# Optimization experiments

Measured on AMD Instinct MI355X. Metric: run time of the kernel, lower is better.

## Reference

```python
import jax, jax.numpy as jnp
import numpy as np
from jax import lax

BN_EPS = 1e-5


def _conv_block(x, w, b):
    # conv k=3 pad=1 (NCHW), relu, maxpool 2x2 stride 2 (floor)
    y = lax.conv_general_dilated(x, w, (1, 1), [(1, 1), (1, 1)],
                                 dimension_numbers=('NCHW', 'OIHW', 'NCHW'))
    y = jax.nn.relu(y + b[None, :, None, None])
    y = lax.reduce_window(y, -jnp.inf, lax.max, (1, 1, 2, 2), (1, 1, 2, 2), 'VALID')
    return y


def _batchnorm_train(x, g, b):
    # BatchNorm2d in train mode: biased batch stats over (N,H,W)
    m = jnp.mean(x, axis=(0, 2, 3), keepdims=True)
    v = jnp.mean(jnp.square(x - m), axis=(0, 2, 3), keepdims=True)
    return g[None, :, None, None] * (x - m) * lax.rsqrt(v + BN_EPS) + b[None, :, None, None]


def setup_inputs() -> dict:
    key = jax.random.key(0)
    ks = jax.random.split(key, 16)
    B = 4096
    s = lambda k, shape, fan: jax.random.normal(k, shape, jnp.float32) * (1.0 / np.sqrt(fan))
    return {
        'x':   jax.random.normal(ks[0], (B, 1, 28, 28), jnp.float32),
        'cw1': s(ks[1], (32, 1, 3, 3), 9),    'cb1': jnp.zeros((32,), jnp.float32),
        'cw2': s(ks[2], (32, 32, 3, 3), 288), 'cb2': jnp.zeros((32,), jnp.float32),
        'cw3': s(ks[3], (32, 32, 3, 3), 288), 'cb3': jnp.zeros((32,), jnp.float32),
        'bn_g': jnp.ones((32,), jnp.float32), 'bn_b': jnp.zeros((32,), jnp.float32),
        'pw1': s(ks[4], (288, 128), 288), 'pb1': jnp.zeros((128,), jnp.float32),
        'pw2': s(ks[5], (128, 128), 128), 'pb2': jnp.zeros((128,), jnp.float32),
        'pw3': s(ks[6], (128, 3), 128),   'pb3': jnp.zeros((3,), jnp.float32),
        'ew1': s(ks[7], (3, 288, 128), 288), 'eb1': jnp.zeros((3, 128), jnp.float32),
        'ew2': s(ks[8], (3, 128, 128), 128), 'eb2': jnp.zeros((3, 128), jnp.float32),
        'ew3': s(ks[9], (3, 128, 10), 128),  'eb3': jnp.zeros((3, 10), jnp.float32),
    }


def _select_linear(h, oh, ew, eb):
    # per-example expert Linear: compute all 3 tiny experts, pick via one-hot
    y = jnp.einsum('bi,eio->beo', h, ew) + eb[None]  # [B,3,out]
    return jnp.einsum('beo,be->bo', y, oh)


def reference(x, cw1, cb1, cw2, cb2, cw3, cb3, bn_g, bn_b,
              pw1, pb1, pw2, pb2, pw3, pb3,
              ew1, eb1, ew2, eb2, ew3, eb3):
    # conv stack
    y = _conv_block(x, cw1, cb1)
    y = _conv_block(y, cw2, cb2)
    y = _conv_block(y, cw3, cb3)
    y = _batchnorm_train(y, bn_g, bn_b)
    y = y.reshape(y.shape[0], -1)  # [B, 288]

    # ActorCritic approx policy MLP (288 -> 128 -> 128 -> 3), greedy action
    h = jax.nn.relu(y @ pw1 + pb1)
    h = jax.nn.relu(h @ pw2 + pb2)
    logits = h @ pw3 + pb3
    actions = jnp.argmax(logits, axis=-1)          # [B] int, routing decision
    oh = jax.nn.one_hot(actions, 3, dtype=y.dtype)  # [B,3]

    # three SelectionLayers, same per-example routing decision
    y = _select_linear(y, oh, ew1, eb1)
    y = _select_linear(y, oh, ew2, eb2)
    y = _select_linear(y, oh, ew3, eb3)  # [B,10]
    return y, actions
```

## Files before the change

### kernel.cpp

```cpp
#include <hip/hip_runtime.h>

__global__ __launch_bounds__(256) void repack_kernel(
    const float* __restrict__ cw2, const float* __restrict__ cw3,
    float* __restrict__ packed2, float* __restrict__ packed3)
{
    int t = blockIdx.x * 256 + threadIdx.x;
    if (t < 9216) {
        int oc = t & 31, r = t >> 5;
        packed2[t] = cw2[oc * 288 + r];
    } else {
        int t2 = t - 9216;
        int oc = t2 & 31, r = t2 >> 5;
        packed3[t2] = cw3[oc * 288 + r];
    }
}

__global__ __launch_bounds__(256)
void fused_conv_kernel(
    const float* __restrict__ x,
    const float* __restrict__ cw1, const float* __restrict__ cb1,
    const float* __restrict__ packed2, const float* __restrict__ cb2,
    const float* __restrict__ packed3, const float* __restrict__ cb3,
    float* __restrict__ out3)
{
    const int img = blockIdx.x;
    const int tid = threadIdx.x;

    __shared__ float A[2304];
    __shared__ float B[10368];
    __shared__ float b2s[32], b3s[32];

    float* xs1 = A;
    float* w1s = A + 900;
    float* b1s = A + 1188;
    float* wck = A;
    float* xs2 = B;
    float* sc  = B;
    float* xs3 = B + 6384;

    for (int i = tid; i < 900;   i += 256) xs1[i] = 0.f;
    for (int i = tid; i < 10368; i += 256) B[i] = 0.f;
    __syncthreads();

    for (int i = tid; i < 784; i += 256) {
        int yy = i / 28, xx = i % 28;
        xs1[(yy + 1) * 30 + xx + 1] = x[img * 784 + i];
    }
    for (int i = tid; i < 288; i += 256) {
        int oc = i & 31, tap = i >> 5;
        w1s[i] = cw1[oc * 9 + tap];
    }
    if (tid < 32) { b1s[tid] = cb1[tid]; b2s[tid] = cb2[tid]; b3s[tid] = cb3[tid]; }
    __syncthreads();

    {
        const int c1 = tid & 31;
        float w1r[9];
        #pragma unroll
        for (int t = 0; t < 9; t++) w1r[t] = w1s[t * 32 + c1];
        const float bias1 = b1s[c1];
        for (int o = tid; o < 32 * 196; o += 256) {
            int p = o >> 5;
            int py = p / 14, px = p % 14;
            int base = (2 * py) * 30 + 2 * px;
            float P[16];
            #pragma unroll
            for (int r = 0; r < 4; r++) {
                float2 u0 = *(const float2*)&xs1[base + r * 30];
                float2 u1 = *(const float2*)&xs1[base + r * 30 + 2];
                P[r * 4 + 0] = u0.x; P[r * 4 + 1] = u0.y;
                P[r * 4 + 2] = u1.x; P[r * 4 + 3] = u1.y;
            }
            float a00 = 0.f, a01 = 0.f, a10 = 0.f, a11 = 0.f;
            #pragma unroll
            for (int ky = 0; ky < 3; ky++)
                #pragma unroll
                for (int kx = 0; kx < 3; kx++) {
                    float w = w1r[ky * 3 + kx];
                    a00 = fmaf(P[ky * 4 + kx],           w, a00);
                    a01 = fmaf(P[ky * 4 + kx + 1],       w, a01);
                    a10 = fmaf(P[(ky + 1) * 4 + kx],     w, a10);
                    a11 = fmaf(P[(ky + 1) * 4 + kx + 1], w, a11);
                }
            float v = fmaxf(fmaxf(fmaxf(a00, a01), fmaxf(a10, a11)) + bias1, 0.f);
            xs2[c1 * 324 + (py + 1) * 20 + (px + 1)] = v;
        }
    }

    const int g  = tid >> 7;
    const int u  = tid & 127;
    const int cb = u & 7, R = u >> 3;
    const int oc0 = cb * 4;
    const bool act2 = (u < 112);

    float acc[4][14];
    #pragma unroll
    for (int a = 0; a < 4; a++)
        #pragma unroll
        for (int c = 0; c < 14; c++) acc[a][c] = 0.f;

    float pf[9];
    #pragma unroll
    for (int k = 0; k < 9; k++) pf[k] = packed2[tid + k * 256];

    for (int ch = 0; ch < 4; ch++) {
        __syncthreads();
        #pragma unroll
        for (int k = 0; k < 9; k++) wck[tid + k * 256] = pf[k];
        if (ch < 3) {
            #pragma unroll
            for (int k = 0; k < 9; k++) pf[k] = packed2[(ch + 1) * 2304 + tid + k * 256];
        }
        __syncthreads();
        if (act2) {
            #pragma unroll 2
            for (int d = 0; d < 4; d++) {
                const int ld = g * 4 + d;
                const int ic = ch * 8 + ld;
                const float* wd = &wck[ld * 288 + oc0];
                const int pb = ic * 324;
                #pragma unroll
                for (int ky = 0; ky < 3; ky++) {
                    const int rb = pb + (R + ky) * 20;
                    float row[16];
                    #pragma unroll
                    for (int q = 0; q < 4; q++) {
                        const float4 t = *(const float4*)&xs2[rb + q * 4];
                        row[q * 4 + 0] = t.x; row[q * 4 + 1] = t.y;
                        row[q * 4 + 2] = t.z; row[q * 4 + 3] = t.w;
                    }
                    const float4 wa = *(const float4*)&wd[(ky * 3 + 0) * 32];
                    const float4 wb = *(const float4*)&wd[(ky * 3 + 1) * 32];
                    const float4 wc = *(const float4*)&wd[(ky * 3 + 2) * 32];
                    #pragma unroll
                    for (int c = 0; c < 14; c++) {
                        acc[0][c] = fmaf(row[c],     wa.x, acc[0][c]);
                        acc[1][c] = fmaf(row[c],     wa.y, acc[1][c]);
                        acc[2][c] = fmaf(row[c],     wa.z, acc[2][c]);
                        acc[3][c] = fmaf(row[c],     wa.w, acc[3][c]);
                        acc[0][c] = fmaf(row[c + 1], wb.x, acc[0][c]);
                        acc[1][c] = fmaf(row[c + 1], wb.y, acc[1][c]);
                        acc[2][c] = fmaf(row[c + 1], wb.z, acc[2][c]);
                        acc[3][c] = fmaf(row[c + 1], wb.w, acc[3][c]);
                        acc[0][c] = fmaf(row[c + 2], wc.x, acc[0][c]);
                        acc[1][c] = fmaf(row[c + 2], wc.y, acc[1][c]);
                        acc[2][c] = fmaf(row[c + 2], wc.z, acc[2][c]);
                        acc[3][c] = fmaf(row[c + 2], wc.w, acc[3][c]);
                    }
                }
            }
        }
    }

    __syncthreads();
    if (g == 1 && act2) {
        #pragma unroll
        for (int a = 0; a < 4; a++)
            #pragma unroll
            for (int c = 0; c < 14; c++) sc[u * 57 + a * 14 + c] = acc[a][c];
    }
    __syncthreads();
    if (g == 0 && act2) {
        #pragma unroll
        for (int a = 0; a < 4; a++)
            #pragma unroll
            for (int c = 0; c < 14; c++) acc[a][c] += sc[u * 57 + a * 14 + c];
    }
    __syncthreads();

    for (int i = tid; i < 2880; i += 256) xs3[i] = 0.f;
    float hm[4][7];
    if (g == 0 && act2) {
        #pragma unroll
        for (int a = 0; a < 4; a++)
            #pragma unroll
            for (int c = 0; c < 7; c++)
                hm[a][c] = fmaxf(acc[a][2 * c], acc[a][2 * c + 1]);
        if (R & 1) {
            #pragma unroll
            for (int a = 0; a < 4; a++)
                #pragma unroll
                for (int c = 0; c < 7; c++) sc[u * 29 + a * 7 + c] = hm[a][c];
        }
    }
    __syncthreads();
    if (g == 0 && act2 && !(R & 1)) {
        const int py = R >> 1;
        #pragma unroll
        for (int a = 0; a < 4; a++)
            #pragma unroll
            for (int c = 0; c < 7; c++) {
                float v = fmaxf(hm[a][c], sc[(u + 8) * 29 + a * 7 + c]);
                v = fmaxf(v + b2s[oc0 + a], 0.f);
                xs3[(oc0 + a) * 90 + (py + 1) * 10 + (c + 1)] = v;
            }
    }

    const int u3 = tid & 127;
    const bool act3 = (u3 < 72);
    const int cq3 = u3 & 7, pos = u3 >> 3;
    const int oc30 = cq3 * 4;
    const int py3 = pos / 3, px3 = pos % 3;
    const int base3 = (2 * py3) * 10 + 2 * px3;

    float a3[4][4];
    #pragma unroll
    for (int a = 0; a < 4; a++)
        #pragma unroll
        for (int q = 0; q < 4; q++) a3[a][q] = 0.f;

    float pg[9];
    #pragma unroll
    for (int k = 0; k < 9; k++) pg[k] = packed3[tid + k * 256];

    for (int ch = 0; ch < 4; ch++) {
        __syncthreads();
        #pragma unroll
        for (int k = 0; k < 9; k++) wck[tid + k * 256] = pg[k];
        if (ch < 3) {
            #pragma unroll
            for (int k = 0; k < 9; k++) pg[k] = packed3[(ch + 1) * 2304 + tid + k * 256];
        }
        __syncthreads();
        if (act3) {
            #pragma unroll 2
            for (int d = 0; d < 4; d++) {
                const int ld = g * 4 + d;
                const int ic = ch * 8 + ld;
                const float* xp = &xs3[ic * 90 + base3];
                float P[16];
                #pragma unroll
                for (int r = 0; r < 4; r++) {
                    float2 u0 = *(const float2*)&xp[r * 10];
                    float2 u1 = *(const float2*)&xp[r * 10 + 2];
                    P[r * 4 + 0] = u0.x; P[r * 4 + 1] = u0.y;
                    P[r * 4 + 2] = u1.x; P[r * 4 + 3] = u1.y;
                }
                const float* wd = &wck[ld * 288 + oc30];
                #pragma unroll
                for (int tap = 0; tap < 9; tap++) {
                    const int ky = tap / 3, kx = tap % 3;
                    const float4 wv = *(const float4*)&wd[tap * 32];
                    const float x00 = P[ky * 4 + kx];
                    const float x01 = P[ky * 4 + kx + 1];
                    const float x10 = P[(ky + 1) * 4 + kx];
                    const float x11 = P[(ky + 1) * 4 + kx + 1];
                    a3[0][0] = fmaf(x00, wv.x, a3[0][0]); a3[0][1] = fmaf(x01, wv.x, a3[0][1]);
                    a3[0][2] = fmaf(x10, wv.x, a3[0][2]); a3[0][3] = fmaf(x11, wv.x, a3[0][3]);
                    a3[1][0] = fmaf(x00, wv.y, a3[1][0]); a3[1][1] = fmaf(x01, wv.y, a3[1][1]);
                    a3[1][2] = fmaf(x10, wv.y, a3[1][2]); a3[1][3] = fmaf(x11, wv.y, a3[1][3]);
                    a3[2][0] = fmaf(x00, wv.z, a3[2][0]); a3[2][1] = fmaf(x01, wv.z, a3[2][1]);
                    a3[2][2] = fmaf(x10, wv.z, a3[2][2]); a3[2][3] = fmaf(x11, wv.z, a3[2][3]);
                    a3[3][0] = fmaf(x00, wv.w, a3[3][0]); a3[3][1] = fmaf(x01, wv.w, a3[3][1]);
                    a3[3][2] = fmaf(x10, wv.w, a3[3][2]); a3[3][3] = fmaf(x11, wv.w, a3[3][3]);
                }
            }
        }
    }

    __syncthreads();
    if (g == 1 && act3) {
        #pragma unroll
        for (int a = 0; a < 4; a++)
            #pragma unroll
            for (int q = 0; q < 4; q++) sc[u3 * 17 + a * 4 + q] = a3[a][q];
    }
    __syncthreads();
    if (g == 0 && act3) {
        #pragma unroll
        for (int a = 0; a < 4; a++)
            #pragma unroll
            for (int q = 0; q < 4; q++) a3[a][q] += sc[u3 * 17 + a * 4 + q];
        float4 res;
        float* r = (float*)&res;
        #pragma unroll
        for (int a = 0; a < 4; a++) {
            float v = fmaxf(fmaxf(a3[a][0], a3[a][1]), fmaxf(a3[a][2], a3[a][3]));
            r[a] = fmaxf(v + b3s[oc30 + a], 0.f);
        }
        *(float4*)&out3[img * 288 + pos * 32 + oc30] = res;
    }
}

__global__ __launch_bounds__(256) void bn_part_kernel(
    const float* __restrict__ out3, float* __restrict__ pS, float* __restrict__ pSS)
{
    const int blk = blockIdx.x;
    const int c = threadIdx.x & 31, ml = threadIdx.x >> 5;
    float s = 0.f, ss = 0.f;
    const int base = blk * 576 + ml;
    for (int k = 0; k < 72; k++) {
        float v = out3[(base + k * 8) * 32 + c];
        s += v; ss = fmaf(v, v, ss);
    }
    __shared__ float rs[256], rss[256];
    rs[threadIdx.x] = s; rss[threadIdx.x] = ss;
    __syncthreads();
    if (threadIdx.x < 32) {
        float S = 0.f, SS = 0.f;
        #pragma unroll
        for (int m = 0; m < 8; m++) { S += rs[threadIdx.x + 32 * m]; SS += rss[threadIdx.x + 32 * m]; }
        pS[blk * 32 + threadIdx.x] = S;
        pSS[blk * 32 + threadIdx.x] = SS;
    }
}

__global__ __launch_bounds__(64) void bn_final_kernel(
    const float* __restrict__ pS, const float* __restrict__ pSS,
    const float* __restrict__ bng, const float* __restrict__ bnb,
    float* __restrict__ stats)
{
    int c = threadIdx.x;
    if (c < 32) {
        float S = 0.f, SS = 0.f;
        for (int b = 0; b < 64; b++) { S += pS[b * 32 + c]; SS += pSS[b * 32 + c]; }
        const float inv_n = 1.f / (4096.f * 9.f);
        float mean = S * inv_n;
        float var = SS * inv_n - mean * mean;
        float a = bng[c] * rsqrtf(var + 1e-5f);
        stats[c] = a;
        stats[32 + c] = bnb[c] - a * mean;
    }
}

__global__ __launch_bounds__(256) void mlp_select_kernel(
    const float* __restrict__ out3, const float* __restrict__ stats,
    const float* __restrict__ pw1, const float* __restrict__ pb1,
    const float* __restrict__ pw2, const float* __restrict__ pb2,
    const float* __restrict__ pw3, const float* __restrict__ pb3,
    const float* __restrict__ ew1, const float* __restrict__ eb1,
    const float* __restrict__ ew2, const float* __restrict__ eb2,
    const float* __restrict__ ew3, const float* __restrict__ eb3,
    float* __restrict__ out)
{
    const int tid = threadIdx.x;
    const int img0 = blockIdx.x * 8;

    __shared__ float ysT[288 * 14];
    __shared__ float hAT[128 * 14];
    __shared__ float hBT[128 * 14];
    __shared__ float lg[24];
    __shared__ int   acts[8];
    __shared__ float sa[32], sb[32];

    if (tid < 32) { sa[tid] = stats[tid]; sb[tid] = stats[32 + tid]; }
    __syncthreads();

    for (int it = 0; it < 3; it++) {
        int i4 = it * 256 + tid;
        if (i4 < 576) {
            int e = i4 / 72, jq = i4 - e * 72;
            float4 v = *(const float4*)&out3[(img0 + e) * 288 + jq * 4];
            int j = jq * 4;
            ysT[(j + 0) * 14 + e] = fmaf(sa[(j + 0) & 31], v.x, sb[(j + 0) & 31]);
            ysT[(j + 1) * 14 + e] = fmaf(sa[(j + 1) & 31], v.y, sb[(j + 1) & 31]);
            ysT[(j + 2) * 14 + e] = fmaf(sa[(j + 2) & 31], v.z, sb[(j + 2) & 31]);
            ysT[(j + 3) * 14 + e] = fmaf(sa[(j + 3) & 31], v.w, sb[(j + 3) & 31]);
        }
    }
    __syncthreads();

    const int n2 = tid & 63, eT = tid >> 6, e0 = eT * 2;
    float acc[2][2];

    #pragma unroll
    for (int e = 0; e < 2; e++) { acc[e][0] = pb1[n2 * 2]; acc[e][1] = pb1[n2 * 2 + 1]; }
    for (int k = 0; k < 288; k++) {
        int i = (k & 31) * 9 + (k >> 5);
        float2 w = *(const float2*)&pw1[i * 128 + n2 * 2];
        float2 yv = *(const float2*)&ysT[k * 14 + e0];
        acc[0][0] = fmaf(yv.x, w.x, acc[0][0]); acc[0][1] = fmaf(yv.x, w.y, acc[0][1]);
        acc[1][0] = fmaf(yv.y, w.x, acc[1][0]); acc[1][1] = fmaf(yv.y, w.y, acc[1][1]);
    }
    #pragma unroll
    for (int e = 0; e < 2; e++)
        #pragma unroll
        for (int d = 0; d < 2; d++)
            hAT[(n2 * 2 + d) * 14 + e0 + e] = fmaxf(acc[e][d], 0.f);
    __syncthreads();

    #pragma unroll
    for (int e = 0; e < 2; e++) { acc[e][0] = pb2[n2 * 2]; acc[e][1] = pb2[n2 * 2 + 1]; }
    for (int k = 0; k < 128; k++) {
        float2 w = *(const float2*)&pw2[k * 128 + n2 * 2];
        float2 hv = *(const float2*)&hAT[k * 14 + e0];
        acc[0][0] = fmaf(hv.x, w.x, acc[0][0]); acc[0][1] = fmaf(hv.x, w.y, acc[0][1]);
        acc[1][0] = fmaf(hv.y, w.x, acc[1][0]); acc[1][1] = fmaf(hv.y, w.y, acc[1][1]);
    }
    #pragma unroll
    for (int e = 0; e < 2; e++)
        #pragma unroll
        for (int d = 0; d < 2; d++)
            hBT[(n2 * 2 + d) * 14 + e0 + e] = fmaxf(acc[e][d], 0.f);
    __syncthreads();

    if (tid < 24) {
        int e = tid / 3, o = tid - e * 3;
        float s = pb3[o];
        for (int k = 0; k < 128; k++) s = fmaf(hBT[k * 14 + e], pw3[k * 3 + o], s);
        lg[e * 3 + o] = s;
    }
    __syncthreads();
    if (tid < 8) {
        float l0 = lg[tid * 3], l1 = lg[tid * 3 + 1], l2 = lg[tid * 3 + 2];
        int a = 0; float best = l0;
        if (l1 > best) { best = l1; a = 1; }
        if (l2 > best) { best = l2; a = 2; }
        acts[tid] = a;
        out[4096 * 10 + img0 + tid] = (float)a;
    }
    __syncthreads();

    const int a0 = acts[e0], a1 = acts[e0 + 1];

    {
        const float* wb0 = ew1 + a0 * 36864;
        const float* wb1 = ew1 + a1 * 36864;
        #pragma unroll
        for (int e = 0; e < 2; e++) { acc[e][0] = 0.f; acc[e][1] = 0.f; }
        for (int k = 0; k < 288; k++) {
            int i = (k & 31) * 9 + (k >> 5);
            float2 wA = *(const float2*)&wb0[i * 128 + n2 * 2];
            float2 wB = *(const float2*)&wb1[i * 128 + n2 * 2];
            float2 yv = *(const float2*)&ysT[k * 14 + e0];
            acc[0][0] = fmaf(yv.x, wA.x, acc[0][0]); acc[0][1] = fmaf(yv.x, wA.y, acc[0][1]);
            acc[1][0] = fmaf(yv.y, wB.x, acc[1][0]); acc[1][1] = fmaf(yv.y, wB.y, acc[1][1]);
        }
        hAT[(n2 * 2 + 0) * 14 + e0 + 0] = acc[0][0] + eb1[a0 * 128 + n2 * 2 + 0];
        hAT[(n2 * 2 + 1) * 14 + e0 + 0] = acc[0][1] + eb1[a0 * 128 + n2 * 2 + 1];
        hAT[(n2 * 2 + 0) * 14 + e0 + 1] = acc[1][0] + eb1[a1 * 128 + n2 * 2 + 0];
        hAT[(n2 * 2 + 1) * 14 + e0 + 1] = acc[1][1] + eb1[a1 * 128 + n2 * 2 + 1];
    }
    __syncthreads();

    {
        const float* wb0 = ew2 + a0 * 16384;
        const float* wb1 = ew2 + a1 * 16384;
        #pragma unroll
        for (int e = 0; e < 2; e++) { acc[e][0] = 0.f; acc[e][1] = 0.f; }
        for (int k = 0; k < 128; k++) {
            float2 wA = *(const float2*)&wb0[k * 128 + n2 * 2];
            float2 wB = *(const float2*)&wb1[k * 128 + n2 * 2];
            float2 hv = *(const float2*)&hAT[k * 14 + e0];
            acc[0][0] = fmaf(hv.x, wA.x, acc[0][0]); acc[0][1] = fmaf(hv.x, wA.y, acc[0][1]);
            acc[1][0] = fmaf(hv.y, wB.x, acc[1][0]); acc[1][1] = fmaf(hv.y, wB.y, acc[1][1]);
        }
        hBT[(n2 * 2 + 0) * 14 + e0 + 0] = acc[0][0] + eb2[a0 * 128 + n2 * 2 + 0];
        hBT[(n2 * 2 + 1) * 14 + e0 + 0] = acc[0][1] + eb2[a0 * 128 + n2 * 2 + 1];
        hBT[(n2 * 2 + 0) * 14 + e0 + 1] = acc[1][0] + eb2[a1 * 128 + n2 * 2 + 0];
        hBT[(n2 * 2 + 1) * 14 + e0 + 1] = acc[1][1] + eb2[a1 * 128 + n2 * 2 + 1];
    }
    __syncthreads();

    if (tid < 80) {
        int e = tid / 10, o = tid - e * 10;
        int a = acts[e];
        float s = eb3[a * 10 + o];
        const float* w3 = &ew3[a * 1280];
        for (int k = 0; k < 128; k++) s = fmaf(hBT[k * 14 + e], w3[k * 10 + o], s);
        out[(img0 + e) * 10 + o] = s;
    }
}

extern "C" void kernel_launch(void* const* d_in, const int* in_sizes, int n_in,
                              void* d_out, int out_size, void* d_ws, size_t ws_size,
                              hipStream_t stream)
{
    const float* x   = (const float*)d_in[0];
    const float* cw1 = (const float*)d_in[1];
    const float* cb1 = (const float*)d_in[2];
    const float* cw2 = (const float*)d_in[3];
    const float* cb2 = (const float*)d_in[4];
    const float* cw3 = (const float*)d_in[5];
    const float* cb3 = (const float*)d_in[6];
    const float* bng = (const float*)d_in[7];
    const float* bnb = (const float*)d_in[8];
    const float* pw1 = (const float*)d_in[9];
    const float* pb1 = (const float*)d_in[10];
    const float* pw2 = (const float*)d_in[11];
    const float* pb2 = (const float*)d_in[12];
    const float* pw3 = (const float*)d_in[13];
    const float* pb3 = (const float*)d_in[14];
    const float* ew1 = (const float*)d_in[15];
    const float* eb1 = (const float*)d_in[16];
    const float* ew2 = (const float*)d_in[17];
    const float* eb2 = (const float*)d_in[18];
    const float* ew3 = (const float*)d_in[19];
    const float* eb3 = (const float*)d_in[20];

    float* out     = (float*)d_out;
    float* out3    = (float*)d_ws;
    float* pS      = out3 + 4096 * 288;
    float* pSS     = pS + 2048;
    float* stats   = pSS + 2048;
    float* packed2 = stats + 64;
    float* packed3 = packed2 + 9216;

    repack_kernel<<<72, 256, 0, stream>>>(cw2, cw3, packed2, packed3);
    fused_conv_kernel<<<4096, 256, 0, stream>>>(x, cw1, cb1, packed2, cb2, packed3, cb3, out3);
    bn_part_kernel<<<64, 256, 0, stream>>>(out3, pS, pSS);
    bn_final_kernel<<<1, 64, 0, stream>>>(pS, pSS, bng, bnb, stats);
    mlp_select_kernel<<<512, 256, 0, stream>>>(out3, stats,
                                               pw1, pb1, pw2, pb2, pw3, pb3,
                                               ew1, eb1, ew2, eb2, ew3, eb3, out);
}
```

Measured before the change: 492.5 us.

## Shrink conv2 LDS footprint with swizzled 16-wide rows and smaller weight chunks

Cuts the padded conv2 input plane from a 20-float to a 16-float row stride and XOR-style rotates the float4 column groups per row to avoid LDS bank conflicts. Weight staging for conv2 now uses 8 chunks of 4 input channels instead of 4 chunks of 8, and conv3 weights and the pooling scratch are relocated into the freed B region. The goal is lower shared memory per block so more blocks can be resident per CU, and fewer bank conflicts. In exchange it adds twice as many barrier rounds in conv2, plus index arithmetic and buffer aliasing that have to stay correct.

```diff
diff --git a/kernel.cpp b/kernel.cpp
--- a/kernel.cpp
+++ b/kernel.cpp
@@ -26,20 +26,22 @@
     const int img = blockIdx.x;
     const int tid = threadIdx.x;
 
-    __shared__ float A[2304];
-    __shared__ float B[10368];
+    __shared__ float A[1220];
+    __shared__ float B[8320];
     __shared__ float b2s[32], b3s[32];
 
-    float* xs1 = A;
-    float* w1s = A + 900;
-    float* b1s = A + 1188;
-    float* wck = A;
-    float* xs2 = B;
-    float* sc  = B;
-    float* xs3 = B + 6384;
-
-    for (int i = tid; i < 900;   i += 256) xs1[i] = 0.f;
-    for (int i = tid; i < 10368; i += 256) B[i] = 0.f;
+    float* xs1  = A;
+    float* w1s  = A + 900;
+    float* b1s  = A + 1188;
+    float* wck2 = A;
+    float* xs2  = B;
+    float* sc   = B;
+    float* xs3  = B + 1280;
+    float* wck3 = B + 4160;
+    float* sc2  = B + 5073;
+
+    for (int i = tid; i < 900;  i += 256) xs1[i] = 0.f;
+    for (int i = tid; i < 8320; i += 256) B[i] = 0.f;
     __syncthreads();
 
     for (int i = tid; i < 784; i += 256) {
@@ -83,7 +85,8 @@
                     a11 = fmaf(P[(ky + 1) * 4 + kx + 1], w, a11);
                 }
             float v = fmaxf(fmaxf(fmaxf(a00, a01), fmaxf(a10, a11)) + bias1, 0.f);
-            xs2[c1 * 324 + (py + 1) * 20 + (px + 1)] = v;
+            int r = py + 1, col = px + 1;
+            xs2[c1 * 260 + r * 16 + ((((col >> 2) + r) & 3) << 2) + (col & 3)] = v;
         }
     }
 
@@ -99,33 +102,43 @@
         #pragma unroll
         for (int c = 0; c < 14; c++) acc[a][c] = 0.f;
 
-    float pf[9];
-    #pragma unroll
-    for (int k = 0; k < 9; k++) pf[k] = packed2[tid + k * 256];
-
-    for (int ch = 0; ch < 4; ch++) {
+    float pf[5];
+    #pragma unroll
+    for (int k = 0; k < 5; k++) {
+        int idx = tid + k * 256;
+        pf[k] = (idx < 1152) ? packed2[idx] : 0.f;
+    }
+
+    for (int ch = 0; ch < 8; ch++) {
         __syncthreads();
         #pragma unroll
-        for (int k = 0; k < 9; k++) wck[tid + k * 256] = pf[k];
-        if (ch < 3) {
-            #pragma unroll
-            for (int k = 0; k < 9; k++) pf[k] = packed2[(ch + 1) * 2304 + tid + k * 256];
+        for (int k = 0; k < 5; k++) {
+            int idx = tid + k * 256;
+            if (idx < 1152) wck2[idx] = pf[k];
+        }
+        if (ch < 7) {
+            #pragma unroll
+            for (int k = 0; k < 5; k++) {
+                int idx = tid + k * 256;
+                pf[k] = (idx < 1152) ? packed2[(ch + 1) * 1152 + idx] : 0.f;
+            }
         }
         __syncthreads();
         if (act2) {
-            #pragma unroll 2
-            for (int d = 0; d < 4; d++) {
-                const int ld = g * 4 + d;
-                const int ic = ch * 8 + ld;
-                const float* wd = &wck[ld * 288 + oc0];
-                const int pb = ic * 324;
+            #pragma unroll
+            for (int d = 0; d < 2; d++) {
+                const int ld = g * 2 + d;
+                const int ic = ch * 4 + ld;
+                const float* wd = &wck2[ld * 288 + oc0];
+                const int pb = ic * 260;
                 #pragma unroll
                 for (int ky = 0; ky < 3; ky++) {
-                    const int rb = pb + (R + ky) * 20;
+                    const int rp = R + ky;
+                    const int rb = pb + rp * 16;
                     float row[16];
                     #pragma unroll
                     for (int q = 0; q < 4; q++) {
-                        const float4 t = *(const float4*)&xs2[rb + q * 4];
+                        const float4 t = *(const float4*)&xs2[rb + (((q + rp) & 3) << 2)];
                         row[q * 4 + 0] = t.x; row[q * 4 + 1] = t.y;
                         row[q * 4 + 2] = t.z; row[q * 4 + 3] = t.w;
                     }
@@ -180,7 +193,7 @@
             #pragma unroll
             for (int a = 0; a < 4; a++)
                 #pragma unroll
-                for (int c = 0; c < 7; c++) sc[u * 29 + a * 7 + c] = hm[a][c];
+                for (int c = 0; c < 7; c++) sc2[u * 29 + a * 7 + c] = hm[a][c];
         }
     }
     __syncthreads();
@@ -190,7 +203,7 @@
         for (int a = 0; a < 4; a++)
             #pragma unroll
             for (int c = 0; c < 7; c++) {
-                float v = fmaxf(hm[a][c], sc[(u + 8) * 29 + a * 7 + c]);
+                float v = fmaxf(hm[a][c], sc2[(u + 8) * 29 + a * 7 + c]);
                 v = fmaxf(v + b2s[oc0 + a], 0.f);
                 xs3[(oc0 + a) * 90 + (py + 1) * 10 + (c + 1)] = v;
             }
@@ -216,7 +229,7 @@
     for (int ch = 0; ch < 4; ch++) {
         __syncthreads();
         #pragma unroll
-        for (int k = 0; k < 9; k++) wck[tid + k * 256] = pg[k];
+        for (int k = 0; k < 9; k++) wck3[tid + k * 256] = pg[k];
         if (ch < 3) {
             #pragma unroll
             for (int k = 0; k < 9; k++) pg[k] = packed3[(ch + 1) * 2304 + tid + k * 256];
@@ -236,7 +249,7 @@
                     P[r * 4 + 0] = u0.x; P[r * 4 + 1] = u0.y;
                     P[r * 4 + 2] = u1.x; P[r * 4 + 3] = u1.y;
                 }
-                const float* wd = &wck[ld * 288 + oc30];
+                const float* wd = &wck3[ld * 288 + oc30];
                 #pragma unroll
                 for (int tap = 0; tap < 9; tap++) {
                     const int ky = tap / 3, kx = tap % 3;
```

Result: faster. 453.4 us (-7.9%).
